# Kernel optimization log

Hardware: AMD Instinct MI355X
Metric: run time of the kernel (lower is better)

The kernel has to match this reference:

```python
import jax, jax.numpy as jnp
import numpy as np

B, S, H = 2, 2048, 1024
NQ, NKV, HD, RANK = 16, 4, 64, 8
THETA = 10000.0
LORA_SCALE = 16 / RANK  # alpha / rank = 2.0
ATTN_SCALE = 1.0 / np.sqrt(HD)


def setup_inputs() -> dict:
    key = jax.random.key(0)
    ks = jax.random.split(key, 14)
    n = lambda k, shape, s: jax.random.normal(k, shape, jnp.float32) * s
    return {
        "x": n(ks[0], (B, S, H), 1.0),
        # nn.Linear weights: [out_features, in_features], y = x @ W.T (scaled small for stability)
        "Wq": n(ks[1], (NQ * HD, H), 0.02),
        "Wk": n(ks[2], (NKV * HD, H), 0.02),
        "Wv": n(ks[3], (NKV * HD, H), 0.02),
        "Wo": n(ks[4], (H, NQ * HD), 0.02),
        "qA": n(ks[5], (RANK, H), 0.05), "qB": n(ks[6], (NQ * HD, RANK), 0.05),
        "kA": n(ks[7], (RANK, H), 0.05), "kB": n(ks[8], (NKV * HD, RANK), 0.05),
        "vA": n(ks[9], (RANK, H), 0.05), "vB": n(ks[10], (NKV * HD, RANK), 0.05),
        "oA": n(ks[11], (RANK, NQ * HD), 0.05), "oB": n(ks[12], (H, RANK), 0.05),
    }


def _lora_proj(x, W, A, Bm):
    # x @ W.T + ((x @ A.T) @ B.T) * lora_scaling
    return x @ W.T + ((x @ A.T) @ Bm.T) * LORA_SCALE


def _rope(x, cos_h, sin_h):
    # x: [b, h, s, d]; even/odd interleaved split, concatenated output (matches torch ref)
    x1, x2 = x[..., ::2], x[..., 1::2]
    return jnp.concatenate([x1 * cos_h - x2 * sin_h, x1 * sin_h + x2 * cos_h], axis=-1)


def _forward(x, Wq, Wk, Wv, Wo, qA, qB, kA, kB, vA, vB, oA, oB):
    b, s, _ = x.shape
    q = _lora_proj(x, Wq, qA, qB).reshape(b, s, NQ, HD).transpose(0, 2, 1, 3)
    k = _lora_proj(x, Wk, kA, kB).reshape(b, s, NKV, HD).transpose(0, 2, 1, 3)
    v = _lora_proj(x, Wv, vA, vB).reshape(b, s, NKV, HD).transpose(0, 2, 1, 3)

    inv_freq = 1.0 / (THETA ** (jnp.arange(0, HD, 2, dtype=jnp.float32) / HD))  # [HD/2]
    freqs = jnp.arange(s, dtype=jnp.float32)[:, None] * inv_freq[None, :]  # [s, HD/2]
    cos_h = jnp.cos(freqs)[None, None]  # [1,1,s,HD/2]
    sin_h = jnp.sin(freqs)[None, None]
    q = _rope(q, cos_h, sin_h)
    k = _rope(k, cos_h, sin_h)

    rep = NQ // NKV  # GQA: repeat_interleave along head axis
    k = jnp.repeat(k, rep, axis=1)
    v = jnp.repeat(v, rep, axis=1)

    attn = jax.nn.softmax(jnp.einsum('bhqd,bhkd->bhqk', q, k) * ATTN_SCALE, axis=-1)
    out = jnp.einsum('bhqk,bhkd->bhqd', attn, v)
    out = out.transpose(0, 2, 1, 3).reshape(b, s, NQ * HD)
    return _lora_proj(out, Wo, oA, oB)


def reference(x, Wq, Wk, Wv, Wo, qA, qB, kA, kB, vA, vB, oA, oB):
    return _forward(x, Wq, Wk, Wv, Wo, qA, qB, kA, kB, vA, vB, oA, oB)
```

## Files before the change

### kernel.cpp

```cpp
#include <hip/hip_runtime.h>

typedef _Float16 f16;
typedef __attribute__((ext_vector_type(8))) _Float16 f16x8;
typedef __attribute__((ext_vector_type(4))) float f32x4;

#define DI __device__ __forceinline__
#define MFMA16(a, b, c) __builtin_amdgcn_mfma_f32_16x16x32_f16(a, b, c, 0, 0, 0)

constexpr int BB = 2, SS = 2048, HH = 1024;
constexpr int NQ = 16, NKV = 4, HD = 64;
constexpr int NTOK = BB * SS;
constexpr int NQKV = NQ*HD + 2*NKV*HD;

DI f32x4 zero4() { f32x4 z = {0.f, 0.f, 0.f, 0.f}; return z; }

DI float fexp2(float x) {
#if __has_builtin(__builtin_amdgcn_exp2f)
  return __builtin_amdgcn_exp2f(x);
#else
  return exp2f(x);
#endif
}

DI unsigned pk2(float a, float b) {
#if __has_builtin(__builtin_amdgcn_cvt_pkrtz)
  typedef __fp16 fp16v2 __attribute__((ext_vector_type(2)));
  union { fp16v2 h; unsigned u; } c;
  c.h = __builtin_amdgcn_cvt_pkrtz(a, b);
  return c.u;
#else
  union { f16 h[2]; unsigned u; } c;
  c.h[0] = (f16)a; c.h[1] = (f16)b; return c.u;
#endif
}

DI void glds16(const void* g, void* l) {
  __builtin_amdgcn_global_load_lds((const __attribute__((address_space(1))) void*)g,
                                   (__attribute__((address_space(3))) void*)l, 16, 0, 0);
}

DI int shuf32(int i) {
  return (i & ~31) | (((i >> 2) & 3) << 3) | (i & 3) | (((i >> 4) & 1) << 2);
}

DI void store4h(f16* dst, float4 v) {
  union { f16 h[4]; uint2 u; } o;
  o.h[0] = (f16)v.x; o.h[1] = (f16)v.y; o.h[2] = (f16)v.z; o.h[3] = (f16)v.w;
  *reinterpret_cast<uint2*>(dst) = o.u;
}

__global__ __launch_bounds__(256) void prep_kernel(
    const float* __restrict__ x,
    const float* __restrict__ Wq, const float* __restrict__ Wk,
    const float* __restrict__ Wv, const float* __restrict__ Wo,
    const float* __restrict__ qA, const float* __restrict__ qB,
    const float* __restrict__ kA, const float* __restrict__ kB,
    const float* __restrict__ vA, const float* __restrict__ vB,
    const float* __restrict__ oA, const float* __restrict__ oB,
    f16* __restrict__ xh, f16* __restrict__ Wqkv, f16* __restrict__ Woe,
    float* __restrict__ ctab, float* __restrict__ stab) {
  int u = blockIdx.x * 256 + threadIdx.x;
  if (u < 393216) {
    int e = u << 2;
    int n = e >> 10, hc = e & 1023;
    const float *Am, *Bm; const float* Wsrc; int nn;
    if (n < 1024)      { nn = n;        Wsrc = Wq + e;              Am = qA; Bm = qB; }
    else if (n < 1280) { nn = n - 1024; Wsrc = Wk + nn*1024 + hc;   Am = kA; Bm = kB; }
    else               { nn = n - 1280; Wsrc = Wv + nn*1024 + hc;   Am = vA; Bm = vB; }
    float4 wv = *reinterpret_cast<const float4*>(Wsrc);
    float4 s = {0.f, 0.f, 0.f, 0.f};
#pragma unroll
    for (int r = 0; r < 8; ++r) {
      float bw = 2.0f * Bm[nn*8 + r];
      float4 av = *reinterpret_cast<const float4*>(Am + r*1024 + hc);
      s.x += bw*av.x; s.y += bw*av.y; s.z += bw*av.z; s.w += bw*av.w;
    }
    wv.x += s.x; wv.y += s.y; wv.z += s.z; wv.w += s.w;
    store4h(Wqkv + shuf32(e), wv);
  } else if ((u -= 393216) < 262144) {
    int e = u << 2;
    int n = e >> 10, hc = e & 1023;
    float4 wv = *reinterpret_cast<const float4*>(Wo + e);
    float4 s = {0.f, 0.f, 0.f, 0.f};
#pragma unroll
    for (int r = 0; r < 8; ++r) {
      float bw = 2.0f * oB[n*8 + r];
      float4 av = *reinterpret_cast<const float4*>(oA + r*1024 + hc);
      s.x += bw*av.x; s.y += bw*av.y; s.z += bw*av.z; s.w += bw*av.w;
    }
    wv.x += s.x; wv.y += s.y; wv.z += s.z; wv.w += s.w;
    store4h(Woe + shuf32(e), wv);
  } else if ((u -= 262144) < 1048576) {
    int e = u << 2;
    float4 v = *reinterpret_cast<const float4*>(x + e);
    store4h(xh + shuf32(e), v);
  } else if ((u -= 1048576) < SS * 32) {
    int s = u >> 5, d = u & 31;
    float inv = expf(-(float)d * 0.28782313662425583f);
    float ang = (float)s * inv;
    ctab[u] = cosf(ang);
    stab[u] = sinf(ang);
  }
}

template<typename OUT_T, int BN>
__global__ __launch_bounds__(256, 2) void gemm_bt(const f16* __restrict__ A, const f16* __restrict__ Bw,
                                                  OUT_T* __restrict__ C, int M, int N, int K) {
  constexpr int BUFB = 16384 + BN * 128;
  __shared__ char lds[2 * BUFB];
  const int nt = N / BN;
  const int nwg = (M >> 7) * nt;
  int bid = blockIdx.x;
  const int cpx = nwg >> 3;
  bid = (bid & 7) * cpx + (bid >> 3);
  const int m0 = (bid / nt) << 7;
  const int n0 = (bid % nt) * BN;
  const int tid = threadIdx.x;
  const int lane = tid & 63;
  const int w = tid >> 6;
  const int wr = (BN == 128) ? (w >> 1) : w;
  const int wc = (BN == 128) ? (w & 1) : 0;
  constexpr int MI = (BN == 128) ? 4 : 2;
  const int l15 = lane & 15, g = (lane >> 4) & 3;
  const char* Ab = (const char*)A;
  const char* Bb = (const char*)Bw;
  const size_t Kb = (size_t)K * 2;
  const int srow = tid >> 3;
  const int scol = (tid & 7) << 4;

  auto stage = [&](int kt, int bs) {
    char* ab = lds + bs * BUFB;
    char* bbuf = ab + 16384;
    const size_t kbyte = (size_t)kt << 7;
#pragma unroll
    for (int s = 0; s < 4; ++s) {
      int row = (s << 5) + srow;
      glds16(Ab + (size_t)(m0 + row) * Kb + kbyte + (scol ^ ((row & 7) << 4)),
             ab + (s << 12) + (w << 10));
    }
#pragma unroll
    for (int s = 0; s < BN / 32; ++s) {
      int row = (s << 5) + srow;
      glds16(Bb + (size_t)(n0 + row) * Kb + kbyte + (scol ^ ((row & 7) << 4)),
             bbuf + (s << 12) + (w << 10));
    }
  };

  f32x4 acc[MI][4];
#pragma unroll
  for (int i = 0; i < MI; ++i)
#pragma unroll
    for (int j = 0; j < 4; ++j) acc[i][j] = zero4();

  const int nkt = K >> 6;
  stage(0, 0);
  for (int t = 0; t < nkt; ++t) {
    __syncthreads();
    if (t + 1 < nkt) stage(t + 1, (t + 1) & 1);
    const char* ab = lds + (t & 1) * BUFB;
    const char* bbuf = ab + 16384;
    f16x8 af[MI][2], bf[4][2];
#pragma unroll
    for (int mi = 0; mi < MI; ++mi) {
      int ra = wr * (MI << 4) + (mi << 4) + l15;
      int base = ra << 7, sw = (ra & 7) << 4;
#pragma unroll
      for (int kk = 0; kk < 2; ++kk)
        af[mi][kk] = *reinterpret_cast<const f16x8*>(ab + base + ((((kk << 6) + (g << 4))) ^ sw));
    }
#pragma unroll
    for (int nj = 0; nj < 4; ++nj) {
      int rb = (wc << 6) + (nj << 4) + l15;
      int base = rb << 7, sw = (rb & 7) << 4;
#pragma unroll
      for (int kk = 0; kk < 2; ++kk)
        bf[nj][kk] = *reinterpret_cast<const f16x8*>(bbuf + base + ((((kk << 6) + (g << 4))) ^ sw));
    }
#pragma unroll
    for (int mi = 0; mi < MI; ++mi)
#pragma unroll
      for (int nj = 0; nj < 4; ++nj) {
        acc[mi][nj] = MFMA16(af[mi][0], bf[nj][0], acc[mi][nj]);
        acc[mi][nj] = MFMA16(af[mi][1], bf[nj][1], acc[mi][nj]);
      }
  }
#pragma unroll
  for (int mi = 0; mi < MI; ++mi)
#pragma unroll
    for (int nj = 0; nj < 4; ++nj) {
      int mmb = m0 + wr * (MI << 4) + (mi << 4) + (g << 2);
      int nn  = n0 + (wc << 6) + (nj << 4) + l15;
      f32x4 a = acc[mi][nj];
#pragma unroll
      for (int r = 0; r < 4; ++r) C[(size_t)(mmb + r) * N + nn] = (OUT_T)a[r];
    }
}

__global__ __launch_bounds__(256) void ropev_kernel(const f16* __restrict__ qkv,
    const float* __restrict__ ctab, const float* __restrict__ stab,
    f16* __restrict__ Qr, f16* __restrict__ Kr, f16* __restrict__ Vt) {
  __shared__ f16 Ls[64 * 72];
  if (blockIdx.x < 10240) {
    int idx = blockIdx.x * 256 + threadIdx.x;
    int dp = idx & 31;
    int t = idx >> 5;
    int hh = t % 20;
    int tok = t / 20;
    int s = tok & (SS - 1), b = tok >> 11;
    float c  = ctab[(s << 5) + dp];
    float sn = stab[(s << 5) + dp];
    const f16* row = qkv + (size_t)tok * NQKV;
    int p1 = (((dp >> 2) & 3) << 3) | (dp & 3) | (((dp >> 4) & 1) << 2);
    if (hh < 16) {
      float x1 = (float)row[hh*64 + 2*dp], x2 = (float)row[hh*64 + 2*dp + 1];
      f16* out = Qr + ((size_t)(b*NQ + hh)*SS + s) * HD;
      constexpr float QS = 0.18033688011112042f;
      out[p1]      = (f16)(QS * (x1*c  - x2*sn));
      out[p1 + 32] = (f16)(QS * (x1*sn + x2*c));
    } else {
      int hk = hh - 16;
      float x1 = (float)row[1024 + hk*64 + 2*dp], x2 = (float)row[1024 + hk*64 + 2*dp + 1];
      f16* out = Kr + ((size_t)(b*NKV + hk)*SS + s) * HD;
      out[p1]      = (f16)(x1*c  - x2*sn);
      out[p1 + 32] = (f16)(x1*sn + x2*c);
    }
  } else {
    const int tid = threadIdx.x;
    const int blk = blockIdx.x - 10240;
    const int st = blk & 31, hkv = (blk >> 5) & 3, b = blk >> 7;
    const int s0 = st << 6;
    {
      int s = tid >> 2, d0 = (tid & 3) << 4;
      const f16* src = qkv + ((size_t)(b*SS + s0 + s)) * NQKV + 1280 + hkv*64 + d0;
      uint4 v0 = *reinterpret_cast<const uint4*>(src);
      uint4 v1 = *reinterpret_cast<const uint4*>(src + 8);
      *reinterpret_cast<uint4*>(Ls + s * 72 + d0) = v0;
      *reinterpret_cast<uint4*>(Ls + s * 72 + d0 + 8) = v1;
    }
    __syncthreads();
    int d = tid >> 2;
    f16* dst = Vt + ((size_t)(b*NKV + hkv)*64 + d) * SS + s0;
#pragma unroll
    for (int cc = 0; cc < 2; ++cc) {
      int cch = ((tid & 3) << 1) + cc;
      int m = cch >> 2, g = cch & 3;
      union { f16 h[8]; uint4 u; } o;
#pragma unroll
      for (int j = 0; j < 8; ++j) {
        int sl = (m << 5) + (g << 2) + (j & 3) + ((j >> 2) << 4);
        o.h[j] = Ls[sl * 72 + d];
      }
      *reinterpret_cast<uint4*>(dst + (cch << 3)) = o.u;
    }
  }
}

__global__ __launch_bounds__(512, 4) void attn_kernel(
    const f16* __restrict__ Qr, const f16* __restrict__ Kr,
    const f16* __restrict__ Vt, f16* __restrict__ AO) {
  __shared__ char lds[3 * 16384];
  const int tid = threadIdx.x, lane = tid & 63, w = tid >> 6;
  const int l15 = lane & 15, g = (lane >> 4) & 3;
  const int bh = blockIdx.x;
  const int b = bh >> 4, h = bh & 15, hkv = h >> 2;
  const int q0 = blockIdx.y << 8;
  const char* Kbase = (const char*)(Kr + (size_t)(b*NKV + hkv) * SS * HD);
  const char* Vbase = (const char*)(Vt + (size_t)(b*NKV + hkv) * HD * SS);

  f16x8 qf[2][2];
  {
    const f16* qr0 = Qr + ((size_t)(b*NQ + h)*SS + q0 + (w << 5) + l15) * HD + (g << 3);
    qf[0][0] = *reinterpret_cast<const f16x8*>(qr0);
    qf[0][1] = *reinterpret_cast<const f16x8*>(qr0 + 32);
    qf[1][0] = *reinterpret_cast<const f16x8*>(qr0 + 16*HD);
    qf[1][1] = *reinterpret_cast<const f16x8*>(qr0 + 16*HD + 32);
  }
  f16x8 ones;
#pragma unroll
  for (int i = 0; i < 8; ++i) ones[i] = (f16)1.0f;
  const f32x4 minit = {-4.f, -4.f, -4.f, -4.f};

  f32x4 acc[4][2];
#pragma unroll
  for (int i = 0; i < 4; ++i) { acc[i][0] = zero4(); acc[i][1] = zero4(); }
  f32x4 es0 = zero4(), es1 = zero4();

  const int srow = tid >> 3;
  const int scolb = (tid & 7) << 4;
  auto stage = [&](int kv0, int buf) {
    char* kb = lds + buf * 16384;
    char* vb = kb + 8192;
    glds16(Kbase + (size_t)(kv0 + srow) * 128 + (scolb ^ ((srow & 7) << 4)),
           kb + (w << 10));
    glds16(Vbase + (size_t)srow * 4096 + (kv0 << 1) + (scolb ^ ((srow & 7) << 4)),
           vb + (w << 10));
  };

  stage(0, 0);
  stage(64, 1);
  int cur = 0;

  for (int t = 0; t < 32; ++t) {
    if (t < 31) asm volatile("s_waitcnt vmcnt(2)" ::: "memory");
    else        asm volatile("s_waitcnt vmcnt(0)" ::: "memory");
    __builtin_amdgcn_s_barrier();
    __builtin_amdgcn_sched_barrier(0);
    int nb = cur + 2; if (nb >= 3) nb -= 3;
    if (t + 2 < 32) stage((t + 2) << 6, nb);

    const char* kb = lds + cur * 16384;
    const char* vb = kb + 8192;

    f32x4 sf0[4], sf1[4];
    __builtin_amdgcn_s_setprio(1);
#pragma unroll
    for (int mb = 0; mb < 4; ++mb) {
      int rowK = (mb << 4) + l15;
      int Bk = (rowK << 7) + ((g << 4) ^ ((rowK & 7) << 4));
      f16x8 kf0 = *reinterpret_cast<const f16x8*>(kb + Bk);
      f16x8 kf1 = *reinterpret_cast<const f16x8*>(kb + (Bk ^ 64));
      f32x4 z0 = minit, z1 = minit;
      z0 = MFMA16(kf0, qf[0][0], z0); z0 = MFMA16(kf1, qf[0][1], z0);
      z1 = MFMA16(kf0, qf[1][0], z1); z1 = MFMA16(kf1, qf[1][1], z1);
      sf0[mb] = z0; sf1[mb] = z1;
    }
    __builtin_amdgcn_s_setprio(0);

    union { unsigned u[8]; f16x8 v[2]; } p0, p1;
#pragma unroll
    for (int j = 0; j < 8; ++j) {
      int mb = j >> 1, r0 = (j & 1) << 1;
      p0.u[j] = pk2(fexp2(sf0[mb][r0]), fexp2(sf0[mb][r0 + 1]));
      p1.u[j] = pk2(fexp2(sf1[mb][r0]), fexp2(sf1[mb][r0 + 1]));
    }

    __builtin_amdgcn_s_setprio(1);
#pragma unroll
    for (int sh = 0; sh < 2; ++sh) {
#pragma unroll
      for (int db = 0; db < 4; ++db) {
        int rowV = (db << 4) + l15;
        int Bv = (rowV << 7) + ((g << 4) ^ ((rowV & 7) << 4));
        f16x8 vf = *reinterpret_cast<const f16x8*>(vb + (Bv ^ (sh << 6)));
        acc[db][0] = MFMA16(vf, p0.v[sh], acc[db][0]);
        acc[db][1] = MFMA16(vf, p1.v[sh], acc[db][1]);
      }
      es0 = MFMA16(ones, p0.v[sh], es0);
      es1 = MFMA16(ones, p1.v[sh], es1);
    }
    __builtin_amdgcn_s_setprio(0);

    cur += 1; if (cur == 3) cur = 0;
  }

  float i0 = 1.0f / es0[0], i1 = 1.0f / es1[0];
  int sg0 = q0 + (w << 5) + l15;
  size_t ob0 = ((size_t)b * SS + sg0) * 1024 + h * 64;
  size_t ob1 = ob0 + (size_t)16 * 1024;
#pragma unroll
  for (int db = 0; db < 4; ++db) {
    union { f16 hv[4]; uint2 u; } o0, o1;
#pragma unroll
    for (int r = 0; r < 4; ++r) {
      o0.hv[r] = (f16)(acc[db][0][r] * i0);
      o1.hv[r] = (f16)(acc[db][1][r] * i1);
    }
    int pos = ((db >> 1) << 5) + (g << 3) + ((db & 1) << 2);
    *reinterpret_cast<uint2*>(AO + ob0 + pos) = o0.u;
    *reinterpret_cast<uint2*>(AO + ob1 + pos) = o1.u;
  }
}

extern "C" void kernel_launch(void* const* d_in, const int* in_sizes, int n_in,
                              void* d_out, int out_size, void* d_ws, size_t ws_size,
                              hipStream_t stream) {
  const float* x  = (const float*)d_in[0];
  const float* Wq = (const float*)d_in[1];
  const float* Wk = (const float*)d_in[2];
  const float* Wv = (const float*)d_in[3];
  const float* Wo = (const float*)d_in[4];
  const float* qA = (const float*)d_in[5];
  const float* qB = (const float*)d_in[6];
  const float* kA = (const float*)d_in[7];
  const float* kB = (const float*)d_in[8];
  const float* vA = (const float*)d_in[9];
  const float* vB = (const float*)d_in[10];
  const float* oA = (const float*)d_in[11];
  const float* oB = (const float*)d_in[12];
  char* ws = (char*)d_ws;
  f16* xh    = (f16*)(ws);
  f16* Wqkv  = (f16*)(ws + 8388608);
  f16* Woe   = (f16*)(ws + 11534336);
  f16* qkv   = (f16*)(ws + 13631488);
  f16* Qr    = (f16*)(ws + 26214400);
  f16* Kr    = (f16*)(ws + 34603008);
  f16* Vt    = (f16*)(ws + 36700160);
  float* ctab = (float*)(ws + 38797312);
  float* stab = (float*)(ws + 39059456);
  f16* AO = xh;
  float* out = (float*)d_out;

  prep_kernel<<<6912, 256, 0, stream>>>(x, Wq, Wk, Wv, Wo, qA, qB, kA, kB, vA, vB, oA, oB,
                                        xh, Wqkv, Woe, ctab, stab);
  gemm_bt<f16, 64><<<dim3(32 * 24), 256, 0, stream>>>(xh, Wqkv, qkv, 4096, 1536, 1024);
  ropev_kernel<<<10496, 256, 0, stream>>>(qkv, ctab, stab, Qr, Kr, Vt);
  attn_kernel<<<dim3(32, 8), 512, 0, stream>>>(Qr, Kr, Vt, AO);
  gemm_bt<float, 64><<<dim3(32 * 16), 256, 0, stream>>>(AO, Woe, out, 4096, 1024, 1024);
}
```

Measured before the change: 88.31 us.

## Vectorize RoPE kernel and software-pipeline PV MFMA across attention iterations

The RoPE part of ropev_kernel now has each thread handle 8 halves with one 16-byte load, float4 cos/sin loads and uint2 stores, so it needs a quarter as many blocks. In the attention kernel, V fragments are read from LDS into registers at the end of each iteration. The P·V MFMAs for the previous tile are then issued at the start of the next iteration, overlapping them with the QK MFMAs and exp. This adds register pressure (vreg plus persistent P) and an epilogue that drains the last tile.

```diff
diff --git a/kernel.cpp b/kernel.cpp
--- a/kernel.cpp
+++ b/kernel.cpp
@@ -200,33 +200,36 @@
     const float* __restrict__ ctab, const float* __restrict__ stab,
     f16* __restrict__ Qr, f16* __restrict__ Kr, f16* __restrict__ Vt) {
   __shared__ f16 Ls[64 * 72];
-  if (blockIdx.x < 10240) {
-    int idx = blockIdx.x * 256 + threadIdx.x;
-    int dp = idx & 31;
-    int t = idx >> 5;
+  if (blockIdx.x < 2560) {
+    int u = blockIdx.x * 256 + threadIdx.x;
+    int j = u & 7;
+    int t = u >> 3;
     int hh = t % 20;
     int tok = t / 20;
     int s = tok & (SS - 1), b = tok >> 11;
-    float c  = ctab[(s << 5) + dp];
-    float sn = stab[(s << 5) + dp];
-    const f16* row = qkv + (size_t)tok * NQKV;
-    int p1 = (((dp >> 2) & 3) << 3) | (dp & 3) | (((dp >> 4) & 1) << 2);
-    if (hh < 16) {
-      float x1 = (float)row[hh*64 + 2*dp], x2 = (float)row[hh*64 + 2*dp + 1];
-      f16* out = Qr + ((size_t)(b*NQ + hh)*SS + s) * HD;
-      constexpr float QS = 0.18033688011112042f;
-      out[p1]      = (f16)(QS * (x1*c  - x2*sn));
-      out[p1 + 32] = (f16)(QS * (x1*sn + x2*c));
-    } else {
-      int hk = hh - 16;
-      float x1 = (float)row[1024 + hk*64 + 2*dp], x2 = (float)row[1024 + hk*64 + 2*dp + 1];
-      f16* out = Kr + ((size_t)(b*NKV + hk)*SS + s) * HD;
-      out[p1]      = (f16)(x1*c  - x2*sn);
-      out[p1 + 32] = (f16)(x1*sn + x2*c);
-    }
+    float4 cs = *reinterpret_cast<const float4*>(ctab + (s << 5) + (j << 2));
+    float4 sn = *reinterpret_cast<const float4*>(stab + (s << 5) + (j << 2));
+    const f16* src = qkv + (size_t)tok * NQKV + (hh < 16 ? hh*64 : 1024 + (hh - 16)*64) + (j << 3);
+    union { uint4 q; f16 h[8]; } v;
+    v.q = *reinterpret_cast<const uint4*>(src);
+    const float sc = hh < 16 ? 0.18033688011112042f : 1.0f;
+    f16* out = (hh < 16) ? (Qr + ((size_t)(b*NQ + hh)*SS + s) * HD)
+                         : (Kr + ((size_t)(b*NKV + hh - 16)*SS + s) * HD);
+    float cc[4] = {cs.x, cs.y, cs.z, cs.w};
+    float ss[4] = {sn.x, sn.y, sn.z, sn.w};
+    union { f16 h[4]; uint2 u2; } o1, o2;
+#pragma unroll
+    for (int e = 0; e < 4; ++e) {
+      float x1 = (float)v.h[2*e], x2 = (float)v.h[2*e + 1];
+      o1.h[e] = (f16)(sc * (x1*cc[e] - x2*ss[e]));
+      o2.h[e] = (f16)(sc * (x1*ss[e] + x2*cc[e]));
+    }
+    int p1b = ((j & 3) << 3) + ((j >> 2) << 2);
+    *reinterpret_cast<uint2*>(out + p1b) = o1.u2;
+    *reinterpret_cast<uint2*>(out + p1b + 32) = o2.u2;
   } else {
     const int tid = threadIdx.x;
-    const int blk = blockIdx.x - 10240;
+    const int blk = blockIdx.x - 2560;
     const int st = blk & 31, hkv = (blk >> 5) & 3, b = blk >> 7;
     const int s0 = st << 6;
     {
@@ -285,6 +288,9 @@
   for (int i = 0; i < 4; ++i) { acc[i][0] = zero4(); acc[i][1] = zero4(); }
   f32x4 es0 = zero4(), es1 = zero4();
 
+  f16x8 vreg[4][2];
+  union { unsigned u[8]; f16x8 v[2]; } p0, p1;
+
   const int srow = tid >> 3;
   const int scolb = (tid & 7) << 4;
   auto stage = [&](int kv0, int buf) {
@@ -311,8 +317,19 @@
     const char* kb = lds + cur * 16384;
     const char* vb = kb + 8192;
 
-    f32x4 sf0[4], sf1[4];
     __builtin_amdgcn_s_setprio(1);
+    if (t > 0) {
+#pragma unroll
+      for (int sh = 0; sh < 2; ++sh) {
+#pragma unroll
+        for (int db = 0; db < 4; ++db) {
+          acc[db][0] = MFMA16(vreg[db][sh], p0.v[sh], acc[db][0]);
+          acc[db][1] = MFMA16(vreg[db][sh], p1.v[sh], acc[db][1]);
+        }
+        es0 = MFMA16(ones, p0.v[sh], es0);
+        es1 = MFMA16(ones, p1.v[sh], es1);
+      }
+    }
 #pragma unroll
     for (int mb = 0; mb < 4; ++mb) {
       int rowK = (mb << 4) + l15;
@@ -322,35 +339,30 @@
       f32x4 z0 = minit, z1 = minit;
       z0 = MFMA16(kf0, qf[0][0], z0); z0 = MFMA16(kf1, qf[0][1], z0);
       z1 = MFMA16(kf0, qf[1][0], z1); z1 = MFMA16(kf1, qf[1][1], z1);
-      sf0[mb] = z0; sf1[mb] = z1;
+      p0.u[(mb << 1)]     = pk2(fexp2(z0[0]), fexp2(z0[1]));
+      p0.u[(mb << 1) + 1] = pk2(fexp2(z0[2]), fexp2(z0[3]));
+      p1.u[(mb << 1)]     = pk2(fexp2(z1[0]), fexp2(z1[1]));
+      p1.u[(mb << 1) + 1] = pk2(fexp2(z1[2]), fexp2(z1[3]));
     }
     __builtin_amdgcn_s_setprio(0);
-
-    union { unsigned u[8]; f16x8 v[2]; } p0, p1;
-#pragma unroll
-    for (int j = 0; j < 8; ++j) {
-      int mb = j >> 1, r0 = (j & 1) << 1;
-      p0.u[j] = pk2(fexp2(sf0[mb][r0]), fexp2(sf0[mb][r0 + 1]));
-      p1.u[j] = pk2(fexp2(sf1[mb][r0]), fexp2(sf1[mb][r0 + 1]));
-    }
-
-    __builtin_amdgcn_s_setprio(1);
-#pragma unroll
-    for (int sh = 0; sh < 2; ++sh) {
-#pragma unroll
-      for (int db = 0; db < 4; ++db) {
-        int rowV = (db << 4) + l15;
-        int Bv = (rowV << 7) + ((g << 4) ^ ((rowV & 7) << 4));
-        f16x8 vf = *reinterpret_cast<const f16x8*>(vb + (Bv ^ (sh << 6)));
-        acc[db][0] = MFMA16(vf, p0.v[sh], acc[db][0]);
-        acc[db][1] = MFMA16(vf, p1.v[sh], acc[db][1]);
-      }
-      es0 = MFMA16(ones, p0.v[sh], es0);
-      es1 = MFMA16(ones, p1.v[sh], es1);
-    }
-    __builtin_amdgcn_s_setprio(0);
-
+#pragma unroll
+    for (int db = 0; db < 4; ++db) {
+      int rowV = (db << 4) + l15;
+      int Bv = (rowV << 7) + ((g << 4) ^ ((rowV & 7) << 4));
+      vreg[db][0] = *reinterpret_cast<const f16x8*>(vb + Bv);
+      vreg[db][1] = *reinterpret_cast<const f16x8*>(vb + (Bv ^ 64));
+    }
     cur += 1; if (cur == 3) cur = 0;
+  }
+#pragma unroll
+  for (int sh = 0; sh < 2; ++sh) {
+#pragma unroll
+    for (int db = 0; db < 4; ++db) {
+      acc[db][0] = MFMA16(vreg[db][sh], p0.v[sh], acc[db][0]);
+      acc[db][1] = MFMA16(vreg[db][sh], p1.v[sh], acc[db][1]);
+    }
+    es0 = MFMA16(ones, p0.v[sh], es0);
+    es1 = MFMA16(ones, p1.v[sh], es1);
   }
 
   float i0 = 1.0f / es0[0], i1 = 1.0f / es1[0];
@@ -403,7 +415,7 @@
   prep_kernel<<<6912, 256, 0, stream>>>(x, Wq, Wk, Wv, Wo, qA, qB, kA, kB, vA, vB, oA, oB,
                                         xh, Wqkv, Woe, ctab, stab);
   gemm_bt<f16, 64><<<dim3(32 * 24), 256, 0, stream>>>(xh, Wqkv, qkv, 4096, 1536, 1024);
-  ropev_kernel<<<10496, 256, 0, stream>>>(qkv, ctab, stab, Qr, Kr, Vt);
+  ropev_kernel<<<2816, 256, 0, stream>>>(qkv, ctab, stab, Qr, Kr, Vt);
   attn_kernel<<<dim3(32, 8), 512, 0, stream>>>(Qr, Kr, Vt, AO);
   gemm_bt<float, 64><<<dim3(32 * 16), 256, 0, stream>>>(AO, Woe, out, 4096, 1024, 1024);
 }
```

Result: faster. 86.22 us (-2.4%).
